# Optimization experiments

Hardware: AMD Instinct MI355X
Metric: run time of the kernel (lower is better)

## Reference

```python
import jax, jax.numpy as jnp
import numpy as np

# static config (matches init_kwargs)
C, NH, WS, H, W, NQ, PS = 384, 12, 8, 56, 56, 64, 8
HD = C // NH
SCALE = HD ** -0.5
EPS = 1e-5
MLP_H = 4 * C


def _rel_pos_index():
    ch, cw = np.meshgrid(np.arange(WS), np.arange(WS), indexing='ij')
    cf = np.stack([ch.ravel(), cw.ravel()])                      # [2, WS*WS]
    rel = cf[:, :, None] - cf[:, None, :]                        # [2, N, N]
    rel = rel.transpose(1, 2, 0)
    rel[:, :, 0] += WS - 1
    rel[:, :, 1] += WS - 1
    rel[:, :, 0] *= 2 * WS - 1
    return jnp.asarray(rel.sum(-1))                              # [N, N] int

REL_IDX = _rel_pos_index()


def _ln(x, g, b):
    mu = x.mean(-1, keepdims=True)
    var = ((x - mu) ** 2).mean(-1, keepdims=True)
    return (x - mu) * jax.lax.rsqrt(var + EPS) * g + b


def setup_inputs() -> dict:
    key = jax.random.key(0)
    ks = jax.random.split(key, 24)
    B = 16
    n = lambda k, shp, s=0.02: jax.random.normal(k, shp, dtype=jnp.float32) * s
    inp = {
        'x': jax.random.normal(ks[0], (B, H * W, C), dtype=jnp.float32),
        'query_tokens': n(ks[1], (1, NQ, C)),
        'kproj_w': n(ks[2], (C, C)), 'kproj_b': jnp.zeros((C,)),
        'kbn_g': jnp.ones((C,)), 'kbn_b': jnp.zeros((C,)),
        'vproj_w': n(ks[3], (C, C)), 'vproj_b': jnp.zeros((C,)),
        'vbn_g': jnp.ones((C,)), 'vbn_b': jnp.zeros((C,)),
        'ck_w': n(ks[4], (C, C)), 'ck_b': jnp.zeros((C,)),
        'cv_w': n(ks[5], (C, C)), 'cv_b': jnp.zeros((C,)),
        'qkv_w': n(ks[6], (C, 3 * C)), 'qkv_b': jnp.zeros((3 * C,)),
        'proj_w': n(ks[7], (C, C)), 'proj_b': jnp.zeros((C,)),
        'rpb_table': n(ks[8], ((2 * WS - 1) ** 2, NH)),
        'norm1_g': jnp.ones((C,)), 'norm1_b': jnp.zeros((C,)),
        'norm2_g': jnp.ones((C,)), 'norm2_b': jnp.zeros((C,)),
        'fc1_w': n(ks[9], (C, MLP_H)), 'fc1_b': jnp.zeros((MLP_H,)),
        'fc2_w': n(ks[10], (MLP_H, C)), 'fc2_b': jnp.zeros((C,)),
    }
    return inp


def _forward(x, query_tokens, kproj_w, kproj_b, kbn_g, kbn_b, vproj_w, vproj_b,
             vbn_g, vbn_b, ck_w, ck_b, cv_w, cv_b, qkv_w, qkv_b, proj_w, proj_b,
             rpb_table, norm1_g, norm1_b, norm2_g, norm2_b, fc1_w, fc1_b, fc2_w, fc2_b):
    B, L, _ = x.shape
    shortcut = x
    xn = _ln(x, norm1_g, norm1_b)                                # [B, L, C]

    # ---- global cross attention (pooled tokens -> learnable queries) ----
    x4 = xn.reshape(B, H, W, C)
    pooled = x4.reshape(B, H // PS, PS, W // PS, PS, C).mean(axis=(2, 4))  # [B,7,7,C]
    pooled = pooled.reshape(B, (H // PS) * (W // PS), C)         # [B, 49, C]
    # conv1x1 + BatchNorm2d (eval mode, default running stats mean=0, var=1)
    bn_scale = 1.0 / jnp.sqrt(1.0 + EPS)
    key = ((pooled @ kproj_w + kproj_b) * bn_scale) * kbn_g + kbn_b
    val = ((pooled @ vproj_w + vproj_b) * bn_scale) * vbn_g + vbn_b

    q = jnp.broadcast_to(query_tokens, (B, NQ, C))
    qh = q.reshape(B, NQ, NH, HD).transpose(0, 2, 1, 3)          # [B,NH,NQ,HD]
    kh = key.reshape(B, -1, NH, HD).transpose(0, 2, 1, 3)
    vh = val.reshape(B, -1, NH, HD).transpose(0, 2, 1, 3)
    attn = jax.nn.softmax(jnp.einsum('bhqd,bhkd->bhqk', qh, kh) * SCALE, axis=-1)
    o = jnp.einsum('bhqk,bhkd->bhqd', attn, vh).transpose(0, 2, 1, 3).reshape(B, NQ, C)
    gk = (o + q) @ ck_w + ck_b                                   # [B, NQ, C]
    gv = (o + q) @ cv_w + cv_b

    # ---- windowed attention with global kv concat ----
    nW = (H // WS) * (W // WS)
    N = WS * WS
    xw = (x4.reshape(B, H // WS, WS, W // WS, WS, C)
             .transpose(0, 1, 3, 2, 4, 5)
             .reshape(B * nW, N, C))                             # [B_, N, C]
    qkv = (xw @ qkv_w + qkv_b).reshape(B * nW, N, 3, NH, HD).transpose(2, 0, 3, 1, 4)
    wq, wk, wv = qkv[0], qkv[1], qkv[2]                          # [B_, NH, N, HD]

    gkh = jnp.broadcast_to(gk.reshape(B, 1, NQ, NH, HD), (B, nW, NQ, NH, HD))
    gkh = gkh.reshape(B * nW, NQ, NH, HD).transpose(0, 2, 1, 3)  # [B_, NH, NQ, HD]
    gvh = jnp.broadcast_to(gv.reshape(B, 1, NQ, NH, HD), (B, nW, NQ, NH, HD))
    gvh = gvh.reshape(B * nW, NQ, NH, HD).transpose(0, 2, 1, 3)
    wk = jnp.concatenate([wk, gkh], axis=2)                      # [B_, NH, N+NQ, HD]
    wv = jnp.concatenate([wv, gvh], axis=2)

    logits = jnp.einsum('bhqd,bhkd->bhqk', wq * SCALE, wk)       # [B_, NH, N, N+NQ]
    rpb = rpb_table[REL_IDX.reshape(-1)].reshape(N, N, NH).transpose(2, 0, 1)  # [NH,N,N]
    logits = logits.at[:, :, :, :N].add(rpb[None])
    wattn = jax.nn.softmax(logits, axis=-1)
    ow = jnp.einsum('bhqk,bhkd->bhqd', wattn, wv).transpose(0, 2, 1, 3).reshape(B * nW, N, C)
    ow = ow @ proj_w + proj_b

    # window reverse
    xr = (ow.reshape(B, H // WS, W // WS, WS, WS, C)
             .transpose(0, 1, 3, 2, 4, 5)
             .reshape(B, H * W, C))

    x = shortcut + xr
    h = jax.nn.gelu(_ln(x, norm2_g, norm2_b) @ fc1_w + fc1_b, approximate=False)
    return x + (h @ fc2_w + fc2_b)


def reference(x, query_tokens, kproj_w, kproj_b, kbn_g, kbn_b, vproj_w, vproj_b,
              vbn_g, vbn_b, ck_w, ck_b, cv_w, cv_b, qkv_w, qkv_b, proj_w, proj_b,
              rpb_table, norm1_g, norm1_b, norm2_g, norm2_b, fc1_w, fc1_b, fc2_w, fc2_b):
    return _forward(x, query_tokens, kproj_w, kproj_b, kbn_g, kbn_b, vproj_w, vproj_b,
                    vbn_g, vbn_b, ck_w, ck_b, cv_w, cv_b, qkv_w, qkv_b, proj_w, proj_b,
                    rpb_table, norm1_g, norm1_b, norm2_g, norm2_b, fc1_w, fc1_b, fc2_w, fc2_b)
```

## Files before the change

kernel.cpp:

```cpp
#include <hip/hip_runtime.h>
#include <math.h>

typedef __attribute__((ext_vector_type(8))) __bf16 bf16x8;
typedef __attribute__((ext_vector_type(4))) float f32x4;
typedef __attribute__((ext_vector_type(8))) unsigned short u16x8;

#define DI __device__ __forceinline__

DI float b2f(unsigned short u) { return __uint_as_float(((unsigned int)u) << 16); }
DI unsigned short f2b(float f) {
    unsigned int x = __float_as_uint(f);
    x += 0x7fffu + ((x >> 16) & 1u);
    return (unsigned short)(x >> 16);
}
DI unsigned short f2b_fast(float f) {
    __bf16 h = (__bf16)f;
    return *(unsigned short*)&h;
}

DI void gl16(const unsigned short* g, unsigned short* l) {
    __builtin_amdgcn_global_load_lds(
        (const __attribute__((address_space(1))) void*)g,
        (__attribute__((address_space(3))) void*)l,
        16, 0, 0);
}

DI float gelu_f(float v) {
    float y = -1.5957691216f * v - 0.0713548163f * v * v * v;
    return v * __builtin_amdgcn_rcpf(1.f + __expf(y));
}

#define SCALE_ATT 0.17677669529663687f
#define BN_SCALE  0.9999950000374997f

__global__ __launch_bounds__(256) void cvt_t_kernel(const float* __restrict__ in,
                                                    unsigned short* __restrict__ out,
                                                    int Kd, int Nd) {
    int i = blockIdx.x * 256 + threadIdx.x;
    if (i < Kd * Nd) {
        int k = i / Nd, n = i % Nd;
        out[(size_t)n * Kd + k] = f2b(in[i]);
    }
}

__global__ __launch_bounds__(64) void ln_kernel(const float* __restrict__ xin,
                                                const float* __restrict__ g,
                                                const float* __restrict__ bsh,
                                                unsigned short* __restrict__ out) {
    int row = blockIdx.x;
    int t = threadIdx.x;
    size_t base = (size_t)row * 384;
    float v[6];
    float s = 0.f;
#pragma unroll
    for (int p = 0; p < 6; ++p) { v[p] = xin[base + t + 64 * p]; s += v[p]; }
#pragma unroll
    for (int off = 32; off > 0; off >>= 1) s += __shfl_xor(s, off);
    float mu = s * (1.f / 384.f);
    float q = 0.f;
#pragma unroll
    for (int p = 0; p < 6; ++p) { float d = v[p] - mu; q += d * d; }
#pragma unroll
    for (int off = 32; off > 0; off >>= 1) q += __shfl_xor(q, off);
    float rstd = rsqrtf(q * (1.f / 384.f) + 1e-5f);
#pragma unroll
    for (int p = 0; p < 6; ++p) {
        int c = t + 64 * p;
        out[base + c] = f2b((v[p] - mu) * rstd * g[c] + bsh[c]);
    }
}

__global__ __launch_bounds__(384) void pool_kernel(const unsigned short* __restrict__ xn,
                                                   float* __restrict__ pooled) {
    int blk = blockIdx.x;
    int b = blk / 49, pp = blk % 49;
    int ph = pp / 7, pw = pp % 7;
    int c = threadIdx.x;
    float s = 0.f;
    for (int i = 0; i < 8; ++i) {
        size_t rb = ((size_t)b * 3136 + (size_t)(ph * 8 + i) * 56 + pw * 8) * 384;
        for (int j = 0; j < 8; ++j) s += b2f(xn[rb + (size_t)j * 384 + c]);
    }
    pooled[(size_t)blk * 384 + c] = s * (1.f / 64.f);
}

__global__ __launch_bounds__(128) void kvproj_kernel(
    const float* __restrict__ pooled,
    const float* __restrict__ kw, const float* __restrict__ kb,
    const float* __restrict__ kg, const float* __restrict__ kbb,
    const float* __restrict__ vw, const float* __restrict__ vb,
    const float* __restrict__ vg, const float* __restrict__ vbb,
    float* __restrict__ keyo, float* __restrict__ valo) {
    __shared__ float row[384];
    int r = blockIdx.x;
    int t = threadIdx.x;
    for (int c = t; c < 384; c += 128) row[c] = pooled[(size_t)r * 384 + c];
    __syncthreads();
#pragma unroll
    for (int p = 0; p < 3; ++p) {
        int c = t + 128 * p;
        float aK = 0.f, aV = 0.f;
        for (int k = 0; k < 384; ++k) {
            float rv = row[k];
            aK += rv * kw[(size_t)k * 384 + c];
            aV += rv * vw[(size_t)k * 384 + c];
        }
        keyo[(size_t)r * 384 + c] = (aK + kb[c]) * BN_SCALE * kg[c] + kbb[c];
        valo[(size_t)r * 384 + c] = (aV + vb[c]) * BN_SCALE * vg[c] + vbb[c];
    }
}

__global__ __launch_bounds__(64) void rpb_expand_kernel(const float* __restrict__ rpbt,
                                                        float* __restrict__ rpb_mat) {
    int h = blockIdx.x >> 6, q = blockIdx.x & 63;
    int k = threadIdx.x;
    int i1 = q >> 3, j1 = q & 7, i2 = k >> 3, j2 = k & 7;
    rpb_mat[((size_t)h * 64 + q) * 64 + k] = rpbt[(size_t)((i1 - i2 + 7) * 15 + (j1 - j2 + 7)) * 12 + h];
}

__global__ __launch_bounds__(64) void cross_attn_kernel(const float* __restrict__ keyg,
                                                        const float* __restrict__ valg,
                                                        const float* __restrict__ qtok,
                                                        float* __restrict__ o) {
    int b = blockIdx.x / 12, h = blockIdx.x % 12;
    __shared__ float kk[49][32];
    __shared__ float vv[49][32];
    int t = threadIdx.x;
    for (int idx = t; idx < 49 * 32; idx += 64) {
        int k = idx >> 5, d = idx & 31;
        size_t gidx = ((size_t)b * 49 + k) * 384 + h * 32 + d;
        kk[k][d] = keyg[gidx];
        vv[k][d] = valg[gidx];
    }
    __syncthreads();
    float q[32];
#pragma unroll
    for (int d = 0; d < 32; ++d) q[d] = qtok[(size_t)t * 384 + h * 32 + d] * SCALE_ATT;
    float lg[49];
    float mx = -1e30f;
#pragma unroll
    for (int k = 0; k < 49; ++k) {
        float s = 0.f;
#pragma unroll
        for (int d = 0; d < 32; ++d) s += q[d] * kk[k][d];
        lg[k] = s;
        mx = fmaxf(mx, s);
    }
    float sum = 0.f;
#pragma unroll
    for (int k = 0; k < 49; ++k) { float e = expf(lg[k] - mx); lg[k] = e; sum += e; }
    float inv = 1.f / sum;
    float od[32];
#pragma unroll
    for (int d = 0; d < 32; ++d) od[d] = 0.f;
#pragma unroll
    for (int k = 0; k < 49; ++k) {
        float wgt = lg[k];
#pragma unroll
        for (int d = 0; d < 32; ++d) od[d] += wgt * vv[k][d];
    }
#pragma unroll
    for (int d = 0; d < 32; ++d) o[((size_t)b * 64 + t) * 384 + h * 32 + d] = od[d] * inv;
}

__global__ __launch_bounds__(128) void gkv_kernel(
    const float* __restrict__ o, const float* __restrict__ qtok,
    const float* __restrict__ ckw, const float* __restrict__ ckb,
    const float* __restrict__ cvw, const float* __restrict__ cvb,
    unsigned short* __restrict__ gk, unsigned short* __restrict__ gv) {
    __shared__ float row[384];
    int r = blockIdx.x;
    int n = r & 63;
    int t = threadIdx.x;
    for (int c = t; c < 384; c += 128)
        row[c] = o[(size_t)r * 384 + c] + qtok[(size_t)n * 384 + c];
    __syncthreads();
#pragma unroll
    for (int p = 0; p < 3; ++p) {
        int c = t + 128 * p;
        float aK = 0.f, aV = 0.f;
        for (int k = 0; k < 384; ++k) {
            float rv = row[k];
            aK += rv * ckw[(size_t)k * 384 + c];
            aV += rv * cvw[(size_t)k * 384 + c];
        }
        gk[(size_t)r * 384 + c] = f2b(aK + ckb[c]);
        gv[(size_t)r * 384 + c] = f2b(aV + cvb[c]);
    }
}

template <int MODE>
__global__ __launch_bounds__(256, 3) void gemm128(const unsigned short* __restrict__ A,
                                                  const unsigned short* __restrict__ BT,
                                                  const float* __restrict__ bias,
                                                  int N, int K,
                                                  void* __restrict__ outp,
                                                  const void* __restrict__ aux0) {
    __shared__ __align__(16) unsigned short As[3][128 * 32];
    __shared__ __align__(16) unsigned short Bs[3][128 * 32];

    int nwg = gridDim.x * gridDim.y;
    int flat = blockIdx.y * gridDim.x + blockIdx.x;
    int flat2 = (flat & 7) * (nwg >> 3) + (flat >> 3);
    int bn = flat2 % gridDim.x, bm = flat2 / gridDim.x;

    int t = threadIdx.x;
    int w = t >> 6, lane = t & 63;
    int wm = w >> 1, wn = w & 1;
    int lo = lane & 15, g = lane >> 4;

    f32x4 acc[4][4];
#pragma unroll
    for (int i = 0; i < 4; ++i)
#pragma unroll
        for (int j = 0; j < 4; ++j) acc[i][j] = f32x4{0.f, 0.f, 0.f, 0.f};

    int srow = w * 32 + (lane >> 2);
    int schunk = (((lane & 3) ^ ((srow >> 1) & 3)) << 3);
    const unsigned short* Ap0 = A + (size_t)(bm * 128 + srow) * K + schunk;
    const unsigned short* Ap1 = A + (size_t)(bm * 128 + srow + 16) * K + schunk;
    const unsigned short* Bp0 = BT + (size_t)(bn * 128 + srow) * K + schunk;
    const unsigned short* Bp1 = BT + (size_t)(bn * 128 + srow + 16) * K + schunk;
    int d0 = (w * 32) * 32, d1 = (w * 32 + 16) * 32;

    int gx = ((g ^ ((lo >> 1) & 3)) << 3);

#define STAGE(buf, kb)                    \
    do {                                  \
        gl16(Ap0 + (kb), As[buf] + d0);   \
        gl16(Ap1 + (kb), As[buf] + d1);   \
        gl16(Bp0 + (kb), Bs[buf] + d0);   \
        gl16(Bp1 + (kb), Bs[buf] + d1);   \
    } while (0)

#define WAIT4() asm volatile("s_waitcnt vmcnt(4)" ::: "memory")
#define WAIT0() asm volatile("s_waitcnt vmcnt(0)" ::: "memory")

#define COMPUTE(buf)                                                                     \
    do {                                                                                 \
        bf16x8 af[4], bfv[4];                                                            \
        _Pragma("unroll")                                                                \
        for (int m = 0; m < 4; ++m)                                                      \
            af[m] = *(const bf16x8*)(As[buf] + (wm * 64 + m * 16 + lo) * 32 + gx);       \
        _Pragma("unroll")                                                                \
        for (int n = 0; n < 4; ++n)                                                      \
            bfv[n] = *(const bf16x8*)(Bs[buf] + (wn * 64 + n * 16 + lo) * 32 + gx);      \
        _Pragma("unroll")                                                                \
        for (int m = 0; m < 4; ++m)                                                      \
            _Pragma("unroll")                                                            \
            for (int n = 0; n < 4; ++n)                                                  \
                acc[m][n] = __builtin_amdgcn_mfma_f32_16x16x32_bf16(af[m], bfv[n],       \
                                                                    acc[m][n], 0, 0, 0); \
    } while (0)

    STAGE(0, 0);
    STAGE(1, 32);

    int nt = K >> 5;
    for (int tt = 0; tt < nt; tt += 3) {
        if (tt + 1 < nt) WAIT4(); else WAIT0();
        __builtin_amdgcn_s_barrier();
        if (tt + 2 < nt) STAGE(2, (tt + 2) * 32);
        COMPUTE(0);
        if (tt + 2 < nt) WAIT4(); else WAIT0();
        __builtin_amdgcn_s_barrier();
        if (tt + 3 < nt) STAGE(0, (tt + 3) * 32);
        COMPUTE(1);
        if (tt + 3 < nt) WAIT4(); else WAIT0();
        __builtin_amdgcn_s_barrier();
        if (tt + 4 < nt) STAGE(1, (tt + 4) * 32);
        COMPUTE(2);
    }
#undef STAGE
#undef WAIT4
#undef WAIT0
#undef COMPUTE

    int r0 = bm * 128 + wm * 64 + g * 4;
    int c0 = bn * 128 + wn * 64 + lo;
    int wgc = bm * 2 + wm;
    int bC = wgc / 49, winC = wgc % 49;
    int whC = winC / 7, wwC = winC % 7;
    int lC = (whC << 3) * 56 + (wwC << 3);
    size_t rowbaseC = (size_t)bC * 3136;
#pragma unroll
    for (int m = 0; m < 4; ++m)
#pragma unroll
        for (int n = 0; n < 4; ++n)
#pragma unroll
            for (int j = 0; j < 4; ++j) {
                int r = r0 + m * 16 + j;
                int c = c0 + n * 16;
                float v = acc[m][n][j] + bias[c];
                if (MODE == 0) {
                    ((unsigned short*)outp)[(size_t)r * N + c] = f2b(v);
                } else if (MODE == 1) {
                    int nn = m * 16 + (g << 2) + j;
                    int l = lC + (nn >> 3) * 56 + (nn & 7);
                    size_t idx = (rowbaseC + l) * 384 + c;
                    ((float*)outp)[idx] = ((const float*)aux0)[idx] + v;
                } else if (MODE == 2) {
                    ((unsigned short*)outp)[(size_t)r * N + c] = f2b(gelu_f(v));
                } else {
                    float res = ((const float*)aux0)[(size_t)r * 384 + c];
                    ((float*)outp)[(size_t)r * N + c] = v + res;
                }
            }
}

__global__ __launch_bounds__(64, 2) void win_attn_mfma(const unsigned short* __restrict__ qkv,
                                                       const unsigned short* __restrict__ gkb,
                                                       const unsigned short* __restrict__ gvb,
                                                       const float* __restrict__ rpb_mat,
                                                       unsigned short* __restrict__ ow) {
    int blk = blockIdx.x;
    int wg = blk / 12, h = blk % 12;
    int b = wg / 49, win = wg % 49;
    int wh = win / 7, ww = win % 7;
    int lane = threadIdx.x;
    int lo = lane & 15, g = lane >> 4;

    __shared__ __align__(16) unsigned short VT[32 * 136];
    __shared__ __align__(16) unsigned short PL[64 * 40];

    size_t qkvbase = (size_t)b * 3136 * 1152;
    int lbase = ((wh << 3)) * 56 + (ww << 3);

    {
        int n = lane;
        int l = lbase + (n >> 3) * 56 + (n & 7);
        const unsigned short* vp = qkv + qkvbase + (size_t)l * 1152 + 768 + h * 32;
        u16x8 v0 = *(const u16x8*)(vp);
        u16x8 v1 = *(const u16x8*)(vp + 8);
        u16x8 v2 = *(const u16x8*)(vp + 16);
        u16x8 v3 = *(const u16x8*)(vp + 24);
#pragma unroll
        for (int j = 0; j < 8; ++j) {
            VT[(0 + j) * 136 + n]  = v0[j];
            VT[(8 + j) * 136 + n]  = v1[j];
            VT[(16 + j) * 136 + n] = v2[j];
            VT[(24 + j) * 136 + n] = v3[j];
        }
        const unsigned short* gp = gvb + ((size_t)b * 64 + n) * 384 + h * 32;
        v0 = *(const u16x8*)(gp);
        v1 = *(const u16x8*)(gp + 8);
        v2 = *(const u16x8*)(gp + 16);
        v3 = *(const u16x8*)(gp + 24);
#pragma unroll
        for (int j = 0; j < 8; ++j) {
            VT[(0 + j) * 136 + 64 + n]  = v0[j];
            VT[(8 + j) * 136 + 64 + n]  = v1[j];
            VT[(16 + j) * 136 + 64 + n] = v2[j];
            VT[(24 + j) * 136 + 64 + n] = v3[j];
        }
    }

    bf16x8 qf[4];
#pragma unroll
    for (int qt = 0; qt < 4; ++qt) {
        int n = qt * 16 + lo;
        int l = lbase + (n >> 3) * 56 + (n & 7);
        qf[qt] = *(const bf16x8*)(qkv + qkvbase + (size_t)l * 1152 + h * 32 + g * 8);
    }

    f32x4 S[4][8];
#pragma unroll
    for (int qt = 0; qt < 4; ++qt)
#pragma unroll
        for (int t = 0; t < 8; ++t) S[qt][t] = f32x4{0.f, 0.f, 0.f, 0.f};

#pragma unroll
    for (int t = 0; t < 8; ++t) {
        bf16x8 kf;
        if (t < 4) {
            int key = t * 16 + lo;
            int l = lbase + (key >> 3) * 56 + (key & 7);
            kf = *(const bf16x8*)(qkv + qkvbase + (size_t)l * 1152 + 384 + h * 32 + g * 8);
        } else {
            int gkey = (t - 4) * 16 + lo;
            kf = *(const bf16x8*)(gkb + ((size_t)b * 64 + gkey) * 384 + h * 32 + g * 8);
        }
#pragma unroll
        for (int qt = 0; qt < 4; ++qt)
            S[qt][t] = __builtin_amdgcn_mfma_f32_16x16x32_bf16(qf[qt], kf, S[qt][t], 0, 0, 0);
    }

    const float* rb_h = rpb_mat + (size_t)h * 4096;
    float mx[4][4];
#pragma unroll
    for (int qt = 0; qt < 4; ++qt)
#pragma unroll
        for (int j = 0; j < 4; ++j) mx[qt][j] = -1e30f;

#pragma unroll
    for (int qt = 0; qt < 4; ++qt) {
#pragma unroll
        for (int t = 0; t < 8; ++t) {
#pragma unroll
            for (int j = 0; j < 4; ++j) {
                float v = S[qt][t][j] * SCALE_ATT;
                if (t < 4) v += rb_h[(qt * 16 + g * 4 + j) * 64 + t * 16 + lo];
                S[qt][t][j] = v;
                mx[qt][j] = fmaxf(mx[qt][j], v);
            }
        }
    }
#pragma unroll
    for (int qt = 0; qt < 4; ++qt)
#pragma unroll
        for (int j = 0; j < 4; ++j) {
#pragma unroll
            for (int m = 1; m <= 8; m <<= 1)
                mx[qt][j] = fmaxf(mx[qt][j], __shfl_xor(mx[qt][j], m));
        }

    float sm[4][4];
#pragma unroll
    for (int qt = 0; qt < 4; ++qt)
#pragma unroll
        for (int j = 0; j < 4; ++j) sm[qt][j] = 0.f;
#pragma unroll
    for (int qt = 0; qt < 4; ++qt)
#pragma unroll
        for (int t = 0; t < 8; ++t)
#pragma unroll
            for (int j = 0; j < 4; ++j) {
                float p = __expf(S[qt][t][j] - mx[qt][j]);
                S[qt][t][j] = p;
                sm[qt][j] += p;
            }
#pragma unroll
    for (int qt = 0; qt < 4; ++qt)
#pragma unroll
        for (int j = 0; j < 4; ++j) {
#pragma unroll
            for (int m = 1; m <= 8; m <<= 1)
                sm[qt][j] += __shfl_xor(sm[qt][j], m);
        }
    float inv[4][4];
#pragma unroll
    for (int qt = 0; qt < 4; ++qt)
#pragma unroll
        for (int j = 0; j < 4; ++j) inv[qt][j] = 1.f / sm[qt][j];

    f32x4 O[4][2];
#pragma unroll
    for (int qt = 0; qt < 4; ++qt)
#pragma unroll
        for (int dt = 0; dt < 2; ++dt) O[qt][dt] = f32x4{0.f, 0.f, 0.f, 0.f};

#pragma unroll
    for (int c = 0; c < 4; ++c) {
        __syncthreads();
#pragma unroll
        for (int qt = 0; qt < 4; ++qt) {
            int qb = qt * 16 + g * 4;
#pragma unroll
            for (int half = 0; half < 2; ++half) {
                int t = 2 * c + half;
#pragma unroll
                for (int j = 0; j < 4; ++j)
                    PL[(qb + j) * 40 + half * 16 + lo] = f2b_fast(S[qt][t][j]);
            }
        }
        __syncthreads();
#pragma unroll
        for (int qt = 0; qt < 4; ++qt) {
            bf16x8 pa = *(const bf16x8*)(PL + (qt * 16 + lo) * 40 + g * 8);
#pragma unroll
            for (int dt = 0; dt < 2; ++dt) {
                bf16x8 vb = *(const bf16x8*)(VT + (dt * 16 + lo) * 136 + c * 32 + g * 8);
                O[qt][dt] = __builtin_amdgcn_mfma_f32_16x16x32_bf16(pa, vb, O[qt][dt], 0, 0, 0);
            }
        }
    }

#pragma unroll
    for (int qt = 0; qt < 4; ++qt)
#pragma unroll
        for (int dt = 0; dt < 2; ++dt)
#pragma unroll
            for (int j = 0; j < 4; ++j) {
                int q = qt * 16 + g * 4 + j;
                int d = dt * 16 + lo;
                ow[((size_t)wg * 64 + q) * 384 + h * 32 + d] = f2b_fast(O[qt][dt][j] * inv[qt][j]);
            }
}

static const size_t OFF_XN   = 0;
static const size_t OFF_QKV  = 38535168;
static const size_t OFF_OW   = 154140672;
static const size_t OFF_X2   = 192675840;
static const size_t OFF_PL   = 269746176;
static const size_t OFF_KEY  = 270950400;
static const size_t OFF_VAL  = 272154624;
static const size_t OFF_O    = 273358848;
static const size_t OFF_GK   = 274931712;
static const size_t OFF_GV   = 276504576;
static const size_t OFF_QKVW = 278077440;
static const size_t OFF_PRJW = 278962176;
static const size_t OFF_FC1W = 279257088;
static const size_t OFF_FC2W = 280436736;

extern "C" void kernel_launch(void* const* d_in, const int* in_sizes, int n_in,
                              void* d_out, int out_size, void* d_ws, size_t ws_size,
                              hipStream_t stream) {
    const float* x      = (const float*)d_in[0];
    const float* qtok   = (const float*)d_in[1];
    const float* kprojw = (const float*)d_in[2];
    const float* kprojb = (const float*)d_in[3];
    const float* kbng   = (const float*)d_in[4];
    const float* kbnb   = (const float*)d_in[5];
    const float* vprojw = (const float*)d_in[6];
    const float* vprojb = (const float*)d_in[7];
    const float* vbng   = (const float*)d_in[8];
    const float* vbnb   = (const float*)d_in[9];
    const float* ckw    = (const float*)d_in[10];
    const float* ckb    = (const float*)d_in[11];
    const float* cvw    = (const float*)d_in[12];
    const float* cvb    = (const float*)d_in[13];
    const float* qkvw   = (const float*)d_in[14];
    const float* qkvb   = (const float*)d_in[15];
    const float* projw  = (const float*)d_in[16];
    const float* projb  = (const float*)d_in[17];
    const float* rpbt   = (const float*)d_in[18];
    const float* n1g    = (const float*)d_in[19];
    const float* n1b    = (const float*)d_in[20];
    const float* n2g    = (const float*)d_in[21];
    const float* n2b    = (const float*)d_in[22];
    const float* fc1w   = (const float*)d_in[23];
    const float* fc1b   = (const float*)d_in[24];
    const float* fc2w   = (const float*)d_in[25];
    const float* fc2b   = (const float*)d_in[26];

    char* wsb = (char*)d_ws;
    unsigned short* xn     = (unsigned short*)(wsb + OFF_XN);
    unsigned short* qkvbf  = (unsigned short*)(wsb + OFF_QKV);
    unsigned short* owbf   = (unsigned short*)(wsb + OFF_OW);
    float* x2      = (float*)(wsb + OFF_X2);
    float* pooled  = (float*)(wsb + OFF_PL);
    float* rpb_mat = (float*)(wsb + OFF_PL);
    float* keyg    = (float*)(wsb + OFF_KEY);
    float* valg    = (float*)(wsb + OFF_VAL);
    float* obuf    = (float*)(wsb + OFF_O);
    unsigned short* gkb = (unsigned short*)(wsb + OFF_GK);
    unsigned short* gvb = (unsigned short*)(wsb + OFF_GV);
    unsigned short* qkvw_t = (unsigned short*)(wsb + OFF_QKVW);
    unsigned short* prjw_t = (unsigned short*)(wsb + OFF_PRJW);
    unsigned short* fc1w_t = (unsigned short*)(wsb + OFF_FC1W);
    unsigned short* fc2w_t = (unsigned short*)(wsb + OFF_FC2W);
    unsigned short* ln2out = (unsigned short*)(wsb + OFF_XN);
    unsigned short* hbuf   = (unsigned short*)(wsb + OFF_QKV);

    cvt_t_kernel<<<(442368 + 255) / 256, 256, 0, stream>>>(qkvw, qkvw_t, 384, 1152);
    cvt_t_kernel<<<(147456 + 255) / 256, 256, 0, stream>>>(projw, prjw_t, 384, 384);
    cvt_t_kernel<<<(589824 + 255) / 256, 256, 0, stream>>>(fc1w, fc1w_t, 384, 1536);
    cvt_t_kernel<<<(589824 + 255) / 256, 256, 0, stream>>>(fc2w, fc2w_t, 1536, 384);
    ln_kernel<<<50176, 64, 0, stream>>>(x, n1g, n1b, xn);
    pool_kernel<<<784, 384, 0, stream>>>(xn, pooled);
    kvproj_kernel<<<784, 128, 0, stream>>>(pooled, kprojw, kprojb, kbng, kbnb,
                                           vprojw, vprojb, vbng, vbnb, keyg, valg);
    rpb_expand_kernel<<<768, 64, 0, stream>>>(rpbt, rpb_mat);
    cross_attn_kernel<<<192, 64, 0, stream>>>(keyg, valg, qtok, obuf);
    gkv_kernel<<<1024, 128, 0, stream>>>(obuf, qtok, ckw, ckb, cvw, cvb, gkb, gvb);
    gemm128<0><<<dim3(9, 392), 256, 0, stream>>>(xn, qkvw_t, qkvb, 1152, 384, qkvbf, nullptr);
    win_attn_mfma<<<9408, 64, 0, stream>>>(qkvbf, gkb, gvb, rpb_mat, owbf);
    gemm128<1><<<dim3(3, 392), 256, 0, stream>>>(owbf, prjw_t, projb, 384, 384, x2, x);
    ln_kernel<<<50176, 64, 0, stream>>>(x2, n2g, n2b, ln2out);
    gemm128<2><<<dim3(12, 392), 256, 0, stream>>>(ln2out, fc1w_t, fc1b, 1536, 384, hbuf, nullptr);
    gemm128<3><<<dim3(3, 392), 256, 0, stream>>>(hbuf, fc2w_t, fc2b, 384, 1536, (float*)d_out, x2);
}
```

Measured before the change: 698.6 us.

## Fuse LayerNorm2, FC1+GELU and FC2+residual into one MLP kernel

```diff
diff --git a/kernel.cpp b/kernel.cpp
--- a/kernel.cpp
+++ b/kernel.cpp
@@ -294,17 +294,142 @@
                 float v = acc[m][n][j] + bias[c];
                 if (MODE == 0) {
                     ((unsigned short*)outp)[(size_t)r * N + c] = f2b(v);
-                } else if (MODE == 1) {
+                } else {
                     int nn = m * 16 + (g << 2) + j;
                     int l = lC + (nn >> 3) * 56 + (nn & 7);
                     size_t idx = (rowbaseC + l) * 384 + c;
                     ((float*)outp)[idx] = ((const float*)aux0)[idx] + v;
-                } else if (MODE == 2) {
-                    ((unsigned short*)outp)[(size_t)r * N + c] = f2b(gelu_f(v));
-                } else {
-                    float res = ((const float*)aux0)[(size_t)r * 384 + c];
-                    ((float*)outp)[(size_t)r * N + c] = v + res;
                 }
+            }
+}
+
+__global__ __launch_bounds__(256, 2) void mlp_fused(const float* __restrict__ x2,
+                                                    const float* __restrict__ n2g,
+                                                    const float* __restrict__ n2b,
+                                                    const unsigned short* __restrict__ W1T,
+                                                    const float* __restrict__ b1v,
+                                                    const unsigned short* __restrict__ W2T,
+                                                    const float* __restrict__ b2v,
+                                                    float* __restrict__ outp) {
+    __shared__ __align__(16) unsigned short As[48 * 32 * 8];
+    __shared__ __align__(16) unsigned short Hs[96 * 32 * 8];
+    __shared__ float muv[32], rsv[32];
+
+    int nwg = gridDim.x;
+    int flat = blockIdx.x;
+    int bm = (flat & 7) * (nwg >> 3) + (flat >> 3);
+    int row0 = bm * 32;
+
+    int t = threadIdx.x;
+    int w = t >> 6, lane = t & 63;
+    int lo = lane & 15, g = lane >> 4;
+
+    {
+        int rl = t >> 3;
+        int c0 = (t & 7) * 48;
+        const float* xp = x2 + (size_t)(row0 + rl) * 384 + c0;
+        float s = 0.f, q = 0.f;
+#pragma unroll
+        for (int i = 0; i < 12; ++i) {
+            f32x4 v = *(const f32x4*)(xp + i * 4);
+#pragma unroll
+            for (int j = 0; j < 4; ++j) { s += v[j]; q += v[j] * v[j]; }
+        }
+#pragma unroll
+        for (int m = 1; m <= 4; m <<= 1) { s += __shfl_xor(s, m); q += __shfl_xor(q, m); }
+        if ((t & 7) == 0) {
+            float mu = s * (1.f / 384.f);
+            muv[rl] = mu;
+            rsv[rl] = rsqrtf(q * (1.f / 384.f) - mu * mu + 1e-5f);
+        }
+    }
+    __syncthreads();
+
+    {
+        int rl = t >> 3;
+        int c0 = (t & 7) * 48;
+        float mu = muv[rl], rs = rsv[rl];
+        const float* xp = x2 + (size_t)(row0 + rl) * 384 + c0;
+#pragma unroll
+        for (int i = 0; i < 6; ++i) {
+            u16x8 pk;
+#pragma unroll
+            for (int j = 0; j < 8; ++j) {
+                int c = c0 + i * 8 + j;
+                pk[j] = f2b((xp[i * 8 + j] - mu) * rs * n2g[c] + n2b[c]);
+            }
+            *(u16x8*)(As + ((size_t)((t & 7) * 6 + i) * 32 + rl) * 8) = pk;
+        }
+    }
+    __syncthreads();
+
+    f32x4 oacc[2][6];
+#pragma unroll
+    for (int m = 0; m < 2; ++m)
+#pragma unroll
+        for (int nf = 0; nf < 6; ++nf) oacc[m][nf] = f32x4{0.f, 0.f, 0.f, 0.f};
+
+    for (int half = 0; half < 2; ++half) {
+#pragma unroll
+        for (int it = 0; it < 3; ++it) {
+            int colb = half * 768 + w * 192 + it * 64;
+            f32x4 hacc[2][4];
+#pragma unroll
+            for (int m = 0; m < 2; ++m)
+#pragma unroll
+                for (int nf = 0; nf < 4; ++nf) hacc[m][nf] = f32x4{0.f, 0.f, 0.f, 0.f};
+            float bb[4];
+#pragma unroll
+            for (int nf = 0; nf < 4; ++nf) bb[nf] = b1v[colb + nf * 16 + lo];
+#pragma unroll
+            for (int ks = 0; ks < 12; ++ks) {
+                bf16x8 a0 = *(const bf16x8*)(As + (((ks * 4 + g) * 32) + lo) * 8);
+                bf16x8 a1 = *(const bf16x8*)(As + (((ks * 4 + g) * 32) + 16 + lo) * 8);
+#pragma unroll
+                for (int nf = 0; nf < 4; ++nf) {
+                    bf16x8 wf = *(const bf16x8*)(W1T + (size_t)(colb + nf * 16 + lo) * 384 + ks * 32 + g * 8);
+                    hacc[0][nf] = __builtin_amdgcn_mfma_f32_16x16x32_bf16(a0, wf, hacc[0][nf], 0, 0, 0);
+                    hacc[1][nf] = __builtin_amdgcn_mfma_f32_16x16x32_bf16(a1, wf, hacc[1][nf], 0, 0, 0);
+                }
+            }
+#pragma unroll
+            for (int m = 0; m < 2; ++m)
+#pragma unroll
+                for (int nf = 0; nf < 4; ++nf) {
+                    int hc = w * 192 + it * 64 + nf * 16 + lo;
+                    unsigned short* hp = Hs + (size_t)(hc >> 3) * 256 + (hc & 7);
+#pragma unroll
+                    for (int j = 0; j < 4; ++j) {
+                        int row = m * 16 + g * 4 + j;
+                        hp[row * 8] = f2b_fast(gelu_f(hacc[m][nf][j] + bb[nf]));
+                    }
+                }
+        }
+        __syncthreads();
+#pragma unroll
+        for (int ks = 0; ks < 24; ++ks) {
+            bf16x8 h0 = *(const bf16x8*)(Hs + (((ks * 4 + g) * 32) + lo) * 8);
+            bf16x8 h1 = *(const bf16x8*)(Hs + (((ks * 4 + g) * 32) + 16 + lo) * 8);
+#pragma unroll
+            for (int nf = 0; nf < 6; ++nf) {
+                bf16x8 wf = *(const bf16x8*)(W2T + (size_t)(w * 96 + nf * 16 + lo) * 1536 + half * 768 + ks * 32 + g * 8);
+                oacc[0][nf] = __builtin_amdgcn_mfma_f32_16x16x32_bf16(h0, wf, oacc[0][nf], 0, 0, 0);
+                oacc[1][nf] = __builtin_amdgcn_mfma_f32_16x16x32_bf16(h1, wf, oacc[1][nf], 0, 0, 0);
+            }
+        }
+        __syncthreads();
+    }
+
+#pragma unroll
+    for (int m = 0; m < 2; ++m)
+#pragma unroll
+        for (int nf = 0; nf < 6; ++nf)
+#pragma unroll
+            for (int j = 0; j < 4; ++j) {
+                int r = row0 + m * 16 + g * 4 + j;
+                int c = w * 96 + nf * 16 + lo;
+                size_t idx = (size_t)r * 384 + c;
+                outp[idx] = oacc[m][nf][j] + b2v[c] + x2[idx];
             }
 }
 
@@ -549,8 +674,6 @@
     unsigned short* prjw_t = (unsigned short*)(wsb + OFF_PRJW);
     unsigned short* fc1w_t = (unsigned short*)(wsb + OFF_FC1W);
     unsigned short* fc2w_t = (unsigned short*)(wsb + OFF_FC2W);
-    unsigned short* ln2out = (unsigned short*)(wsb + OFF_XN);
-    unsigned short* hbuf   = (unsigned short*)(wsb + OFF_QKV);
 
     cvt_t_kernel<<<(442368 + 255) / 256, 256, 0, stream>>>(qkvw, qkvw_t, 384, 1152);
     cvt_t_kernel<<<(147456 + 255) / 256, 256, 0, stream>>>(projw, prjw_t, 384, 384);
@@ -566,7 +689,5 @@
     gemm128<0><<<dim3(9, 392), 256, 0, stream>>>(xn, qkvw_t, qkvb, 1152, 384, qkvbf, nullptr);
     win_attn_mfma<<<9408, 64, 0, stream>>>(qkvbf, gkb, gvb, rpb_mat, owbf);
     gemm128<1><<<dim3(3, 392), 256, 0, stream>>>(owbf, prjw_t, projb, 384, 384, x2, x);
-    ln_kernel<<<50176, 64, 0, stream>>>(x2, n2g, n2b, ln2out);
-    gemm128<2><<<dim3(12, 392), 256, 0, stream>>>(ln2out, fc1w_t, fc1b, 1536, 384, hbuf, nullptr);
-    gemm128<3><<<dim3(3, 392), 256, 0, stream>>>(hbuf, fc2w_t, fc2b, 384, 1536, (float*)d_out, x2);
-}
+    mlp_fused<<<1568, 256, 0, stream>>>(x2, n2g, n2b, fc1w_t, fc1b, fc2w_t, fc2b, (float*)d_out);
+}
```

Measured after the change: 1.150 ms. 64.6% more time.

## Make QKV and FC1 GEMMs persistent with cross-tile prefetch pipelining

Applied to the files above, without the earlier changes.

```diff
diff --git a/kernel.cpp b/kernel.cpp
--- a/kernel.cpp
+++ b/kernel.cpp
@@ -188,50 +188,6 @@
         gv[(size_t)r * 384 + c] = f2b(aV + cvb[c]);
     }
 }
-
-template <int MODE>
-__global__ __launch_bounds__(256, 3) void gemm128(const unsigned short* __restrict__ A,
-                                                  const unsigned short* __restrict__ BT,
-                                                  const float* __restrict__ bias,
-                                                  int N, int K,
-                                                  void* __restrict__ outp,
-                                                  const void* __restrict__ aux0) {
-    __shared__ __align__(16) unsigned short As[3][128 * 32];
-    __shared__ __align__(16) unsigned short Bs[3][128 * 32];
-
-    int nwg = gridDim.x * gridDim.y;
-    int flat = blockIdx.y * gridDim.x + blockIdx.x;
-    int flat2 = (flat & 7) * (nwg >> 3) + (flat >> 3);
-    int bn = flat2 % gridDim.x, bm = flat2 / gridDim.x;
-
-    int t = threadIdx.x;
-    int w = t >> 6, lane = t & 63;
-    int wm = w >> 1, wn = w & 1;
-    int lo = lane & 15, g = lane >> 4;
-
-    f32x4 acc[4][4];
-#pragma unroll
-    for (int i = 0; i < 4; ++i)
-#pragma unroll
-        for (int j = 0; j < 4; ++j) acc[i][j] = f32x4{0.f, 0.f, 0.f, 0.f};
-
-    int srow = w * 32 + (lane >> 2);
-    int schunk = (((lane & 3) ^ ((srow >> 1) & 3)) << 3);
-    const unsigned short* Ap0 = A + (size_t)(bm * 128 + srow) * K + schunk;
-    const unsigned short* Ap1 = A + (size_t)(bm * 128 + srow + 16) * K + schunk;
-    const unsigned short* Bp0 = BT + (size_t)(bn * 128 + srow) * K + schunk;
-    const unsigned short* Bp1 = BT + (size_t)(bn * 128 + srow + 16) * K + schunk;
-    int d0 = (w * 32) * 32, d1 = (w * 32 + 16) * 32;
-
-    int gx = ((g ^ ((lo >> 1) & 3)) << 3);
-
-#define STAGE(buf, kb)                    \
-    do {                                  \
-        gl16(Ap0 + (kb), As[buf] + d0);   \
-        gl16(Ap1 + (kb), As[buf] + d1);   \
-        gl16(Bp0 + (kb), Bs[buf] + d0);   \
-        gl16(Bp1 + (kb), Bs[buf] + d1);   \
-    } while (0)
 
 #define WAIT4() asm volatile("s_waitcnt vmcnt(4)" ::: "memory")
 #define WAIT0() asm volatile("s_waitcnt vmcnt(0)" ::: "memory")
@@ -253,6 +209,50 @@
                                                                     acc[m][n], 0, 0, 0); \
     } while (0)
 
+template <int MODE>
+__global__ __launch_bounds__(256, 3) void gemm128(const unsigned short* __restrict__ A,
+                                                  const unsigned short* __restrict__ BT,
+                                                  const float* __restrict__ bias,
+                                                  int N, int K,
+                                                  void* __restrict__ outp,
+                                                  const void* __restrict__ aux0) {
+    __shared__ __align__(16) unsigned short As[3][128 * 32];
+    __shared__ __align__(16) unsigned short Bs[3][128 * 32];
+
+    int nwg = gridDim.x * gridDim.y;
+    int flat = blockIdx.y * gridDim.x + blockIdx.x;
+    int flat2 = (flat & 7) * (nwg >> 3) + (flat >> 3);
+    int bn = flat2 % gridDim.x, bm = flat2 / gridDim.x;
+
+    int t = threadIdx.x;
+    int w = t >> 6, lane = t & 63;
+    int wm = w >> 1, wn = w & 1;
+    int lo = lane & 15, g = lane >> 4;
+
+    f32x4 acc[4][4];
+#pragma unroll
+    for (int i = 0; i < 4; ++i)
+#pragma unroll
+        for (int j = 0; j < 4; ++j) acc[i][j] = f32x4{0.f, 0.f, 0.f, 0.f};
+
+    int srow = w * 32 + (lane >> 2);
+    int schunk = (((lane & 3) ^ ((srow >> 1) & 3)) << 3);
+    const unsigned short* Ap0 = A + (size_t)(bm * 128 + srow) * K + schunk;
+    const unsigned short* Ap1 = A + (size_t)(bm * 128 + srow + 16) * K + schunk;
+    const unsigned short* Bp0 = BT + (size_t)(bn * 128 + srow) * K + schunk;
+    const unsigned short* Bp1 = BT + (size_t)(bn * 128 + srow + 16) * K + schunk;
+    int d0 = (w * 32) * 32, d1 = (w * 32 + 16) * 32;
+
+    int gx = ((g ^ ((lo >> 1) & 3)) << 3);
+
+#define STAGE(buf, kb)                    \
+    do {                                  \
+        gl16(Ap0 + (kb), As[buf] + d0);   \
+        gl16(Ap1 + (kb), As[buf] + d1);   \
+        gl16(Bp0 + (kb), Bs[buf] + d0);   \
+        gl16(Bp1 + (kb), Bs[buf] + d1);   \
+    } while (0)
+
     STAGE(0, 0);
     STAGE(1, 32);
 
@@ -272,9 +272,6 @@
         COMPUTE(2);
     }
 #undef STAGE
-#undef WAIT4
-#undef WAIT0
-#undef COMPUTE
 
     int r0 = bm * 128 + wm * 64 + g * 4;
     int c0 = bn * 128 + wn * 64 + lo;
@@ -292,20 +289,115 @@
                 int r = r0 + m * 16 + j;
                 int c = c0 + n * 16;
                 float v = acc[m][n][j] + bias[c];
-                if (MODE == 0) {
-                    ((unsigned short*)outp)[(size_t)r * N + c] = f2b(v);
-                } else if (MODE == 1) {
+                if (MODE == 1) {
                     int nn = m * 16 + (g << 2) + j;
                     int l = lC + (nn >> 3) * 56 + (nn & 7);
                     size_t idx = (rowbaseC + l) * 384 + c;
                     ((float*)outp)[idx] = ((const float*)aux0)[idx] + v;
-                } else if (MODE == 2) {
-                    ((unsigned short*)outp)[(size_t)r * N + c] = f2b(gelu_f(v));
                 } else {
                     float res = ((const float*)aux0)[(size_t)r * 384 + c];
                     ((float*)outp)[(size_t)r * N + c] = v + res;
                 }
             }
+}
+
+struct P4 { const unsigned short *a0, *a1, *b0, *b1; };
+DI P4 mkptr(const unsigned short* A, const unsigned short* BT, int idx, int NB, int K,
+            int srow, int schunk) {
+    int bm = idx / NB, bn = idx - bm * NB;
+    P4 p;
+    p.a0 = A + (size_t)(bm * 128 + srow) * K + schunk;
+    p.a1 = p.a0 + (size_t)16 * K;
+    p.b0 = BT + (size_t)(bn * 128 + srow) * K + schunk;
+    p.b1 = p.b0 + (size_t)16 * K;
+    return p;
+}
+DI void stage4(P4 p, unsigned short* AsB, unsigned short* BsB, int d0, int d1, int kb) {
+    gl16(p.a0 + kb, AsB + d0);
+    gl16(p.a1 + kb, AsB + d1);
+    gl16(p.b0 + kb, BsB + d0);
+    gl16(p.b1 + kb, BsB + d1);
+}
+
+template <int MODE>
+__global__ __launch_bounds__(256, 3) void gemm128p(const unsigned short* __restrict__ A,
+                                                   const unsigned short* __restrict__ BT,
+                                                   const float* __restrict__ bias,
+                                                   int N, int K, int NB, int chunk, int Ttot,
+                                                   unsigned short* __restrict__ outp) {
+    __shared__ __align__(16) unsigned short As[3][128 * 32];
+    __shared__ __align__(16) unsigned short Bs[3][128 * 32];
+
+    int nblk = gridDim.x;
+    int b = blockIdx.x;
+    int bsw = (b & 7) * (nblk >> 3) + (b >> 3);
+    int i0 = bsw * chunk;
+    if (i0 >= Ttot) return;
+    int i1 = i0 + chunk;
+    if (i1 > Ttot) i1 = Ttot;
+
+    int t = threadIdx.x;
+    int w = t >> 6, lane = t & 63;
+    int wm = w >> 1, wn = w & 1;
+    int lo = lane & 15, g = lane >> 4;
+
+    int srow = w * 32 + (lane >> 2);
+    int schunk = (((lane & 3) ^ ((srow >> 1) & 3)) << 3);
+    int d0 = (w * 32) * 32, d1 = (w * 32 + 16) * 32;
+    int gx = ((g ^ ((lo >> 1) & 3)) << 3);
+    int nt = K >> 5;
+    int total = (i1 - i0) * nt;
+
+    P4 cur = mkptr(A, BT, i0, NB, K, srow, schunk);
+    P4 nxt = (i0 + 1 < i1) ? mkptr(A, BT, i0 + 1, NB, K, srow, schunk) : cur;
+
+    stage4(cur, As[0], Bs[0], d0, d1, 0);
+    stage4(cur, As[1], Bs[1], d0, d1, 32);
+
+    int kt = 0, bufc = 0;
+    for (int idx = i0; idx < i1; ++idx) {
+        f32x4 acc[4][4];
+#pragma unroll
+        for (int i = 0; i < 4; ++i)
+#pragma unroll
+            for (int j = 0; j < 4; ++j) acc[i][j] = f32x4{0.f, 0.f, 0.f, 0.f};
+
+        for (int lt = 0; lt < nt; ++lt, ++kt) {
+            if (kt + 1 < total) WAIT4(); else WAIT0();
+            __builtin_amdgcn_s_barrier();
+            if (kt + 2 < total) {
+                int slt = lt + 2;
+                P4 sp = cur;
+                if (slt >= nt) { slt -= nt; sp = nxt; }
+                int sb = bufc + 2; if (sb >= 3) sb -= 3;
+                stage4(sp, As[sb], Bs[sb], d0, d1, slt * 32);
+            }
+            COMPUTE(bufc);
+            bufc = (bufc == 2) ? 0 : bufc + 1;
+        }
+
+        int bm = idx / NB, bn = idx - bm * NB;
+        int r0 = bm * 128 + wm * 64 + g * 4;
+        int c0 = bn * 128 + wn * 64 + lo;
+#pragma unroll
+        for (int m = 0; m < 4; ++m)
+#pragma unroll
+            for (int n = 0; n < 4; ++n)
+#pragma unroll
+                for (int j = 0; j < 4; ++j) {
+                    int r = r0 + m * 16 + j;
+                    int c = c0 + n * 16;
+                    float v = acc[m][n][j] + bias[c];
+                    if (MODE == 0) {
+                        outp[(size_t)r * N + c] = f2b(v);
+                    } else {
+                        outp[(size_t)r * N + c] = f2b(gelu_f(v));
+                    }
+                }
+
+        cur = nxt;
+        nxt = (idx + 2 < i1) ? mkptr(A, BT, idx + 2, NB, K, srow, schunk) : cur;
+    }
 }
 
 __global__ __launch_bounds__(64, 2) void win_attn_mfma(const unsigned short* __restrict__ qkv,
@@ -563,10 +655,10 @@
     rpb_expand_kernel<<<768, 64, 0, stream>>>(rpbt, rpb_mat);
     cross_attn_kernel<<<192, 64, 0, stream>>>(keyg, valg, qtok, obuf);
     gkv_kernel<<<1024, 128, 0, stream>>>(obuf, qtok, ckw, ckb, cvw, cvb, gkb, gvb);
-    gemm128<0><<<dim3(9, 392), 256, 0, stream>>>(xn, qkvw_t, qkvb, 1152, 384, qkvbf, nullptr);
+    gemm128p<0><<<888, 256, 0, stream>>>(xn, qkvw_t, qkvb, 1152, 384, 9, 4, 3528, qkvbf);
     win_attn_mfma<<<9408, 64, 0, stream>>>(qkvbf, gkb, gvb, rpb_mat, owbf);
     gemm128<1><<<dim3(3, 392), 256, 0, stream>>>(owbf, prjw_t, projb, 384, 384, x2, x);
     ln_kernel<<<50176, 64, 0, stream>>>(x2, n2g, n2b, ln2out);
-    gemm128<2><<<dim3(12, 392), 256, 0, stream>>>(ln2out, fc1w_t, fc1b, 1536, 384, hbuf, nullptr);
+    gemm128p<2><<<784, 256, 0, stream>>>(ln2out, fc1w_t, fc1b, 1536, 384, 12, 6, 4704, hbuf);
     gemm128<3><<<dim3(3, 392), 256, 0, stream>>>(hbuf, fc2w_t, fc2b, 384, 1536, (float*)d_out, x2);
 }
```

New measurement: 766.0 us. 9.7% more time.
